# Performance work log

Hardware: AMD Instinct MI355X
Metric: run time of the kernel (lower is better)

The kernel has to match this reference:

```python
import jax, jax.numpy as jnp
import numpy as np

B, S, D, H = 2, 2048, 2048, 16
HD = D // H  # 128
ROPE_BASE = 10000.0


def _rope_tables(seq_len, head_dim, dtype=jnp.float32):
    inv_freq = 1.0 / (ROPE_BASE ** (jnp.arange(0, head_dim, 2, dtype=jnp.float32) / head_dim))
    t = jnp.arange(seq_len, dtype=jnp.float32)
    freqs = jnp.outer(t, inv_freq)  # [S, HD/2]
    # broadcast shape [1, S, 1, HD/2]
    return jnp.cos(freqs)[None, :, None, :].astype(dtype), jnp.sin(freqs)[None, :, None, :].astype(dtype)


def _apply_rope(x, cos, sin):
    # x: [B, S, H, HD]; interleaved split, output concatenated by halves (matches torch code)
    x1 = x[..., ::2]
    x2 = x[..., 1::2]
    return jnp.concatenate([x1 * cos - x2 * sin, x1 * sin + x2 * cos], axis=-1)


def setup_inputs() -> dict:
    key = jax.random.key(0)
    ks = jax.random.split(key, 9)
    xavier = lambda k: jax.random.uniform(k, (D, D), jnp.float32, -1.0, 1.0) * np.sqrt(6.0 / (D + D))
    return {
        "x": jax.random.normal(ks[0], (B, S, D), jnp.float32),
        "attention_mask": jnp.ones((B, S), jnp.int32),
        "wq": xavier(ks[1]), "bq": jnp.zeros((D,), jnp.float32),
        "wk": xavier(ks[2]), "bk": jnp.zeros((D,), jnp.float32),
        "wv": xavier(ks[3]), "bv": jnp.zeros((D,), jnp.float32),
        "wo": xavier(ks[4]), "bo": jnp.zeros((D,), jnp.float32),
    }


def reference(x, attention_mask, wq, bq, wk, bk, wv, bv, wo, bo):
    b, s, _ = x.shape
    scale = HD ** -0.5
    q = (x @ wq + bq).reshape(b, s, H, HD)
    k = (x @ wk + bk).reshape(b, s, H, HD)
    v = (x @ wv + bv).reshape(b, s, H, HD)
    cos, sin = _rope_tables(s, HD, x.dtype)
    q = _apply_rope(q, cos, sin)
    k = _apply_rope(k, cos, sin)
    # [B, H, S, S]
    scores = jnp.einsum('bqhd,bkhd->bhqk', q, k) * scale
    mask = attention_mask[:, None, None, :]  # 2D mask -> [B,1,1,S]
    scores = jnp.where(mask == 0, jnp.asarray(-1e9, scores.dtype), scores)
    attn = jax.nn.softmax(scores, axis=-1)
    out = jnp.einsum('bhqk,bkhd->bqhd', attn, v).reshape(b, s, D)
    return out @ wo + bo
```

## Files before the change

kernel.cpp:

```cpp
#include <hip/hip_runtime.h>

#define Bc 2
#define Sc 2048
#define Dc 2048
#define Hc 16
#define HDc 128
#define Mc 4096

typedef __bf16 bf16_t;
typedef __bf16 bf16x4 __attribute__((ext_vector_type(4)));
typedef __bf16 bf16x8 __attribute__((ext_vector_type(8)));
typedef float f32x4 __attribute__((ext_vector_type(4)));
typedef float f32x16 __attribute__((ext_vector_type(16)));

__device__ __forceinline__ f32x4 mfma16(bf16x8 a, bf16x8 b, f32x4 c) {
  return __builtin_amdgcn_mfma_f32_16x16x32_bf16(a, b, c, 0, 0, 0);
}
__device__ __forceinline__ f32x16 mfma32(bf16x8 a, bf16x8 b, f32x16 c) {
  return __builtin_amdgcn_mfma_f32_32x32x16_bf16(a, b, c, 0, 0, 0);
}

typedef const unsigned __attribute__((address_space(1))) gu32_t;
typedef unsigned __attribute__((address_space(3))) lu32_t;

__device__ __forceinline__ void gload_lds16(const void* g, void* l) {
  gu32_t* gp = (gu32_t*)(unsigned long long)g;
  lu32_t* lp = (lu32_t*)(unsigned)(unsigned long long)l;
  __builtin_amdgcn_global_load_lds(gp, lp, 16, 0, 0);
}

__device__ __forceinline__ unsigned cvtpk(float lo, float hi_) {
  unsigned r;
  asm("v_cvt_pk_bf16_f32 %0, %1, %2" : "=v"(r) : "v"(lo), "v"(hi_));
  return r;
}
__device__ __forceinline__ void plswap(unsigned& a, unsigned& b) {
  asm volatile("v_permlane32_swap_b32 %0, %1" : "+v"(a), "+v"(b));
}

__global__ void cvt_bf16_kernel(const float* __restrict__ in, bf16_t* __restrict__ out, int n4) {
  int i = blockIdx.x * blockDim.x + threadIdx.x;
  if (i < n4) {
    float4 v = ((const float4*)in)[i];
    bf16x4 o;
    o[0] = (bf16_t)v.x; o[1] = (bf16_t)v.y; o[2] = (bf16_t)v.z; o[3] = (bf16_t)v.w;
    ((bf16x4*)out)[i] = o;
  }
}

__global__ void rope_table_kernel(float2* __restrict__ tbl) {
  const int s = blockIdx.x, j = threadIdx.x;
  float freq = expf(-(float)j * (9.210340371976184f / 64.0f));
  float ang = (float)s * freq;
  float sn, cs;
  sincosf(ang, &sn, &cs);
  tbl[s * 64 + j] = make_float2(cs, sn);
}

__global__ void transpose_cvt4_kernel(const float* __restrict__ w0, const float* __restrict__ w1,
                                      const float* __restrict__ w2, const float* __restrict__ w3,
                                      bf16_t* __restrict__ dqkv, bf16_t* __restrict__ dwo) {
  __shared__ float tile[32][33];
  const int z = blockIdx.z;
  const float* w = z == 0 ? w0 : (z == 1 ? w1 : (z == 2 ? w2 : w3));
  bf16_t* wt = z < 3 ? dqkv + (size_t)z * Dc * Dc : dwo;
  const int tx = threadIdx.x, ty = threadIdx.y;
  const int n0 = blockIdx.x * 32, k0 = blockIdx.y * 32;
#pragma unroll
  for (int i = 0; i < 32; i += 8)
    tile[ty + i][tx] = w[(size_t)(k0 + ty + i) * Dc + n0 + tx];
  __syncthreads();
#pragma unroll
  for (int i = 0; i < 32; i += 8)
    wt[(size_t)(n0 + ty + i) * Dc + k0 + tx] = (bf16_t)tile[tx][ty + i];
}

template <int MODE, int NT8>
__global__ __launch_bounds__(512, 1) void gemmp_kernel(
    const bf16_t* __restrict__ A, const bf16_t* __restrict__ Bt,
    const float* __restrict__ bias0, const float* __restrict__ bias1,
    const float* __restrict__ bias2, const float2* __restrict__ tbl,
    void* __restrict__ out0, void* __restrict__ out1, void* __restrict__ out2) {
  __shared__ __align__(16) bf16_t sA[3][256 * 64];
  __shared__ __align__(16) bf16_t sB[3][128 * 64];
  const int tid = threadIdx.x;
  const int lane = tid & 63, wid = tid >> 6;
  const int l15 = lane & 15, g = lane >> 4;
  const int wrow = wid >> 1, wcol = wid & 1;

  const int nwg = 16 * NT8, cpx = nwg / 8;
  const int wgid = ((int)blockIdx.x & 7) * cpx + ((int)blockIdx.x >> 3);
  const int nt = wgid % NT8, mt = wgid / NT8;
  const int m0 = mt * 256, n0 = nt * 128;

  const bf16_t* Ab = A + (size_t)m0 * 2048;
  const bf16_t* Bb = Bt + (size_t)n0 * 2048;

#define GP_STAGE_A(kt, i_)                                           \
  {                                                                  \
    int s_ = (i_) * 512 + tid;                                       \
    int r_ = s_ >> 3;                                                \
    int c_ = ((s_ & 7) ^ (r_ & 7)) * 8;                              \
    gload_lds16(Ab + (size_t)r_ * 2048 + (kt) * 64 + c_,             \
                (char*)&sA[(kt) % 3][0] + s_ * 16);                  \
  }
#define GP_STAGE_B(kt, i_)                                           \
  {                                                                  \
    int s_ = (i_) * 512 + tid;                                       \
    int r_ = s_ >> 3;                                                \
    int c_ = ((s_ & 7) ^ (r_ & 7)) * 8;                              \
    gload_lds16(Bb + (size_t)r_ * 2048 + (kt) * 64 + c_,             \
                (char*)&sB[(kt) % 3][0] + s_ * 16);                  \
  }

  f32x4 acc[4][4] = {};

  GP_STAGE_A(0, 0) GP_STAGE_A(0, 1) GP_STAGE_A(0, 2) GP_STAGE_A(0, 3)
  GP_STAGE_B(0, 0) GP_STAGE_B(0, 1)
  GP_STAGE_A(1, 0) GP_STAGE_A(1, 1) GP_STAGE_A(1, 2) GP_STAGE_A(1, 3)
  GP_STAGE_B(1, 0) GP_STAGE_B(1, 1)

#define GP_BODY(t, DOSTG, VMSTR)                                               \
  {                                                                            \
    asm volatile("s_waitcnt vmcnt(" VMSTR ")" ::: "memory");                   \
    __builtin_amdgcn_s_barrier();                                              \
    __builtin_amdgcn_sched_barrier(0);                                         \
    const char* pA = (const char*)&sA[(t) % 3][0];                             \
    const char* pB = (const char*)&sB[(t) % 3][0];                             \
    bf16x8 af[4][2], bf0[2][2], bf1[2][2];                                     \
    _Pragma("unroll") for (int mi = 0; mi < 4; ++mi)                           \
        _Pragma("unroll") for (int ks = 0; ks < 2; ++ks) {                     \
      int r = wrow * 64 + mi * 16 + l15;                                       \
      af[mi][ks] = *(const bf16x8*)(pA + r * 128 + (((ks * 4 + g) ^ (r & 7)) * 16)); \
    }                                                                          \
    _Pragma("unroll") for (int ni = 0; ni < 2; ++ni)                           \
        _Pragma("unroll") for (int ks = 0; ks < 2; ++ks) {                     \
      int r = wcol * 64 + ni * 16 + l15;                                       \
      bf0[ni][ks] = *(const bf16x8*)(pB + r * 128 + (((ks * 4 + g) ^ (r & 7)) * 16)); \
    }                                                                          \
    if (DOSTG) { GP_STAGE_A((t) + 2, 0) GP_STAGE_A((t) + 2, 1) GP_STAGE_B((t) + 2, 0) } \
    __builtin_amdgcn_s_setprio(1);                                             \
    _Pragma("unroll") for (int mi = 0; mi < 4; ++mi)                           \
        _Pragma("unroll") for (int ni = 0; ni < 2; ++ni)                       \
            _Pragma("unroll") for (int ks = 0; ks < 2; ++ks)                   \
                acc[mi][ni] = mfma16(af[mi][ks], bf0[ni][ks], acc[mi][ni]);    \
    __builtin_amdgcn_s_setprio(0);                                             \
    __builtin_amdgcn_s_barrier();                                              \
    __builtin_amdgcn_sched_barrier(0);                                         \
    _Pragma("unroll") for (int ni = 0; ni < 2; ++ni)                           \
        _Pragma("unroll") for (int ks = 0; ks < 2; ++ks) {                     \
      int r = wcol * 64 + (ni + 2) * 16 + l15;                                 \
      bf1[ni][ks] = *(const bf16x8*)(pB + r * 128 + (((ks * 4 + g) ^ (r & 7)) * 16)); \
    }                                                                          \
    if (DOSTG) { GP_STAGE_A((t) + 2, 2) GP_STAGE_A((t) + 2, 3) GP_STAGE_B((t) + 2, 1) } \
    __builtin_amdgcn_s_setprio(1);                                             \
    _Pragma("unroll") for (int mi = 0; mi < 4; ++mi)                           \
        _Pragma("unroll") for (int ni = 0; ni < 2; ++ni)                       \
            _Pragma("unroll") for (int ks = 0; ks < 2; ++ks)                   \
                acc[mi][ni + 2] = mfma16(af[mi][ks], bf1[ni][ks], acc[mi][ni + 2]); \
    __builtin_amdgcn_s_setprio(0);                                             \
  }

  for (int t = 0; t < 30; ++t) GP_BODY(t, 1, "6");
  GP_BODY(30, 0, "6");
  GP_BODY(31, 0, "0");

#undef GP_BODY
#undef GP_STAGE_A
#undef GP_STAGE_B

  if (MODE == 2) {
#pragma unroll
    for (int mi = 0; mi < 4; ++mi) {
#pragma unroll
      for (int ni = 0; ni < 4; ++ni) {
        const int ncol = n0 + wcol * 64 + ni * 16 + l15;
        const float bv = bias0[ncol];
#pragma unroll
        for (int r = 0; r < 4; ++r) {
          const int mrow = m0 + wrow * 64 + mi * 16 + g * 4 + r;
          ((float*)out0)[(size_t)mrow * 2048 + ncol] = acc[mi][ni][r] + bv;
        }
      }
    }
  } else {
    const int proj = n0 >> 11;
    const float* bp = proj == 0 ? bias0 : (proj == 1 ? bias1 : bias2);
    bf16_t* op = (bf16_t*)(proj == 0 ? out0 : (proj == 1 ? out1 : out2));
#pragma unroll
    for (int mi = 0; mi < 4; ++mi) {
#pragma unroll
      for (int ni = 0; ni < 4; ++ni) {
        const int ncol = n0 + wcol * 64 + ni * 16 + l15;
        const int nloc = ncol & 2047;
        const float bv = bp[nloc];
        const int h = nloc >> 7, hd = nloc & 127;
        if (proj < 2) {
          const int j = hd >> 1;
#pragma unroll
          for (int r = 0; r < 4; ++r) {
            const int mrow = m0 + wrow * 64 + mi * 16 + g * 4 + r;
            const int b = mrow >> 11, sq = mrow & 2047;
            float vv = acc[mi][ni][r] + bv;
            float part = __shfl_xor(vv, 1);
            float2 cn = tbl[(size_t)sq * 64 + j];
            float ov = (l15 & 1) ? (part * cn.y + vv * cn.x)
                                 : (vv * cn.x - part * cn.y);
            op[(((size_t)(b * Hc + h) * Sc + sq) * HDc) + hd] = (bf16_t)ov;
          }
        } else {
#pragma unroll
          for (int r = 0; r < 4; ++r) {
            const int mrow = m0 + wrow * 64 + mi * 16 + g * 4 + r;
            const int b = mrow >> 11, sq = mrow & 2047;
            const float v = acc[mi][ni][r] + bv;
            op[(((size_t)(b * Hc + h) * HDc + hd) * Sc) + sq] = (bf16_t)v;
          }
        }
      }
    }
  }
}

__global__ __launch_bounds__(256, 2) void attn_kernel(
    const bf16_t* __restrict__ Q, const bf16_t* __restrict__ Kr,
    const bf16_t* __restrict__ Vt, const int* __restrict__ mask,
    bf16_t* __restrict__ AO) {
  __shared__ __align__(16) bf16_t sK[2][64 * 128];
  __shared__ __align__(16) bf16_t sV[2][64 * 128];
  __shared__ float mbias[Sc];
  __shared__ float bcast[4][32];
  const int tid = threadIdx.x;
  const int w = tid >> 6, lane = tid & 63;
  const int l31 = lane & 31, hi = lane >> 5;
  const int wbase = w * 64;

  const int bid = blockIdx.x;
  const int L = ((bid & 7) << 6) + (bid >> 3);
  const int qc = L & 15, h = (L >> 4) & 15, b = L >> 8;

  const int* mb = mask + b * Sc;
#pragma unroll
  for (int i = 0; i < Sc / 256; ++i)
    mbias[i * 256 + tid] = mb[i * 256 + tid] ? 0.f : -1e9f;

  const int q0 = qc * 128 + w * 32;
  const bf16_t* qb = Q + ((size_t)(b * Hc + h) * Sc + q0) * HDc;
  const bf16_t* kb = Kr + ((size_t)(b * Hc + h) * Sc) * HDc;
  const bf16_t* vb = Vt + ((size_t)(b * Hc + h) * HDc) * Sc;

  bf16x8 qf[8];
  {
    const bf16_t* qr = qb + (size_t)l31 * HDc + hi * 8;
#pragma unroll
    for (int kk = 0; kk < 8; ++kk) qf[kk] = *(const bf16x8*)(qr + kk * 16);
  }

#define STAGE_KV(sKb, sVb, kv0_)                                             \
  {                                                                          \
    _Pragma("unroll") for (int p = 0; p < 4; ++p) {                          \
      int s_ = p * 256 + tid;                                                \
      int rk = s_ >> 4, ck = s_ & 15;                                        \
      gload_lds16(kb + (size_t)((kv0_) + rk) * HDc + ((ck ^ (rk & 15)) * 8), \
                  (char*)(sKb) + (size_t)(p * 256 + wbase) * 16);            \
      int d63 = s_ >> 4, sv = s_ & 15;                                       \
      int tmp = sv ^ (d63 & 15);                                             \
      int hb = tmp >> 3, cv = tmp & 7;                                       \
      gload_lds16(vb + (size_t)(hb * 64 + d63) * Sc + (kv0_) + cv * 8,       \
                  (char*)(sVb) + (size_t)(p * 256 + wbase) * 16);            \
    }                                                                        \
  }

  bf16_t* sKc = &sK[0][0];
  bf16_t* sKn = &sK[1][0];
  bf16_t* sVc = &sV[0][0];
  bf16_t* sVn = &sV[1][0];

  STAGE_KV(sKc, sVc, 0);
  asm volatile("s_waitcnt vmcnt(0)" ::: "memory");
  __syncthreads();

  f32x16 acc[4];
#pragma unroll
  for (int d = 0; d < 4; ++d) acc[d] = 0.f;
  float mrun = -3.0e38f, lrun = 0.f;
  const float scale = 0.08838834764831845f;

  for (int kv0 = 0; kv0 < Sc; kv0 += 64) {
    if (kv0 + 64 < Sc) STAGE_KV(sKn, sVn, kv0 + 64);

    f32x16 s0 = 0.f, s1 = 0.f;
    {
      const char* kbase = (const char*)sKc;
      __builtin_amdgcn_s_setprio(1);
#pragma unroll
      for (int kk = 0; kk < 8; ++kk) {
        bf16x8 k0f = *(const bf16x8*)(kbase + l31 * 256 + (((2 * kk + hi) ^ (l31 & 15)) * 16));
        bf16x8 k1f = *(const bf16x8*)(kbase + (32 + l31) * 256 + (((2 * kk + hi) ^ ((32 + l31) & 15)) * 16));
        s0 = mfma32(k0f, qf[kk], s0);
        s1 = mfma32(k1f, qf[kk], s1);
      }
      __builtin_amdgcn_s_setprio(0);
    }
    float v[32];
    {
      const float* mp = mbias + kv0 + 4 * hi;
#pragma unroll
      for (int g4 = 0; g4 < 4; ++g4) {
        f32x4 b0 = *(const f32x4*)(mp + 8 * g4);
        f32x4 b1 = *(const f32x4*)(mp + 32 + 8 * g4);
#pragma unroll
        for (int j = 0; j < 4; ++j) {
          v[g4 * 4 + j] = s0[g4 * 4 + j] * scale + b0[j];
          v[16 + g4 * 4 + j] = s1[g4 * 4 + j] * scale + b1[j];
        }
      }
    }
    float tm = v[0];
#pragma unroll
    for (int r = 1; r < 32; ++r) tm = fmaxf(tm, v[r]);
    tm = fmaxf(tm, __shfl_xor(tm, 32));
    if (__any(tm > mrun + 8.f)) {
      float mnew = fmaxf(mrun, tm);
      float al = __expf(mrun - mnew);
      mrun = mnew;
      lrun *= al;
      bcast[w][l31] = al;
      asm volatile("s_waitcnt lgkmcnt(0)" ::: "memory");
      __builtin_amdgcn_sched_barrier(0);
#pragma unroll
      for (int g4 = 0; g4 < 4; ++g4) {
        f32x4 alr = *(const f32x4*)(&bcast[w][8 * g4 + 4 * hi]);
#pragma unroll
        for (int dblk = 0; dblk < 4; ++dblk)
#pragma unroll
          for (int j = 0; j < 4; ++j) acc[dblk][g4 * 4 + j] *= alr[j];
      }
    }
    float ts = 0.f;
#pragma unroll
    for (int r = 0; r < 32; ++r) {
      v[r] = __expf(v[r] - mrun);
      ts += v[r];
    }
    ts += __shfl_xor(ts, 32);
    lrun += ts;
    unsigned pk[4][4];
#pragma unroll
    for (int ks = 0; ks < 4; ++ks) {
      unsigned a1 = cvtpk(v[ks * 8 + 0], v[ks * 8 + 1]);
      unsigned b1 = cvtpk(v[ks * 8 + 4], v[ks * 8 + 5]);
      unsigned a2 = cvtpk(v[ks * 8 + 2], v[ks * 8 + 3]);
      unsigned b2 = cvtpk(v[ks * 8 + 6], v[ks * 8 + 7]);
      plswap(a1, b1);
      plswap(a2, b2);
      pk[ks][0] = a1; pk[ks][1] = a2; pk[ks][2] = b1; pk[ks][3] = b2;
    }
    {
      const char* vbase = (const char*)sVc;
      __builtin_amdgcn_s_setprio(1);
#pragma unroll
      for (int ks = 0; ks < 4; ++ks) {
        bf16x8 pa = *(const bf16x8*)&pk[ks][0];
#pragma unroll
        for (int dblk = 0; dblk < 4; ++dblk) {
          int d = dblk * 32 + l31;
          int slot = (((d >> 6) * 8 + (2 * ks + hi)) ^ (d & 15));
          bf16x8 vf = *(const bf16x8*)(vbase + (d & 63) * 256 + slot * 16);
          acc[dblk] = mfma32(pa, vf, acc[dblk]);
        }
      }
      __builtin_amdgcn_s_setprio(0);
    }
    asm volatile("s_waitcnt vmcnt(0)" ::: "memory");
    __syncthreads();
    bf16_t* t1 = sKc; sKc = sKn; sKn = t1;
    bf16_t* t2 = sVc; sVc = sVn; sVn = t2;
  }

  float inv = 1.f / lrun;
  bcast[w][l31] = inv;
  asm volatile("s_waitcnt lgkmcnt(0)" ::: "memory");
  __builtin_amdgcn_sched_barrier(0);
  bf16_t* ob = AO + ((size_t)b * Sc + q0) * Dc + h * HDc;
#pragma unroll
  for (int g4 = 0; g4 < 4; ++g4) {
    f32x4 ir = *(const f32x4*)(&bcast[w][8 * g4 + 4 * hi]);
#pragma unroll
    for (int j = 0; j < 4; ++j) {
      int q = 8 * g4 + 4 * hi + j;
#pragma unroll
      for (int dblk = 0; dblk < 4; ++dblk)
        ob[(size_t)q * Dc + dblk * 32 + l31] = (bf16_t)(acc[dblk][g4 * 4 + j] * ir[j]);
    }
  }
}

#define MB(x) ((size_t)(x) << 20)

extern "C" void kernel_launch(void* const* d_in, const int* in_sizes, int n_in,
                              void* d_out, int out_size, void* d_ws, size_t ws_size,
                              hipStream_t stream) {
  const float* x = (const float*)d_in[0];
  const int* mask = (const int*)d_in[1];
  const float* wq = (const float*)d_in[2];
  const float* bq = (const float*)d_in[3];
  const float* wk = (const float*)d_in[4];
  const float* bk = (const float*)d_in[5];
  const float* wv = (const float*)d_in[6];
  const float* bv = (const float*)d_in[7];
  const float* wo = (const float*)d_in[8];
  const float* bo = (const float*)d_in[9];
  float* out = (float*)d_out;

  char* ws = (char*)d_ws;
  bf16_t* xb     = (bf16_t*)(ws + MB(0));
  bf16_t* wqkvT  = (bf16_t*)(ws + MB(16));
  bf16_t* woT    = (bf16_t*)(ws + MB(40));
  bf16_t* qbuf   = (bf16_t*)(ws + MB(48));
  bf16_t* kbuf   = (bf16_t*)(ws + MB(64));
  bf16_t* vtb    = (bf16_t*)(ws + MB(80));
  bf16_t* ao     = (bf16_t*)(ws + MB(96));
  float2* rtbl   = (float2*)(ws + MB(112));

  cvt_bf16_kernel<<<8192, 256, 0, stream>>>(x, xb, (Mc * Dc) / 4);
  rope_table_kernel<<<Sc, 64, 0, stream>>>(rtbl);

  dim3 tg(64, 64, 4), tb(32, 8);
  transpose_cvt4_kernel<<<tg, tb, 0, stream>>>(wq, wk, wv, wo, wqkvT, woT);

  gemmp_kernel<0, 48><<<768, 512, 0, stream>>>(xb, wqkvT, bq, bk, bv, rtbl, qbuf, kbuf, vtb);

  attn_kernel<<<Bc * Hc * (Sc / 128), 256, 0, stream>>>(qbuf, kbuf, vtb, mask, ao);

  gemmp_kernel<2, 16><<<256, 512, 0, stream>>>(ao, woT, bo, bo, bo, rtbl, out, out, out);
}
```

Baseline: 270.3 us.

## Process 64 query rows per wave in attention to reuse K/V fragments

Each wave now handles two 32-row query sub-tiles, with two sets of accumulators and separate online-softmax state, so every K and V fragment read from LDS feeds twice as many MFMAs. The block covers 256 queries, which halves the grid and halves the total K/V global and LDS traffic. Launch bounds drop to one block per CU to allow the larger register footprint. The cost is lower occupancy and fewer blocks (256) across the CUs, which reduces latency hiding and may leave some CUs idle.

```diff
diff --git a/kernel.cpp b/kernel.cpp
--- a/kernel.cpp
+++ b/kernel.cpp
@@ -222,7 +222,7 @@
   }
 }
 
-__global__ __launch_bounds__(256, 2) void attn_kernel(
+__global__ __launch_bounds__(256, 1) void attn_kernel(
     const bf16_t* __restrict__ Q, const bf16_t* __restrict__ Kr,
     const bf16_t* __restrict__ Vt, const int* __restrict__ mask,
     bf16_t* __restrict__ AO) {
@@ -236,24 +236,28 @@
   const int wbase = w * 64;
 
   const int bid = blockIdx.x;
-  const int L = ((bid & 7) << 6) + (bid >> 3);
-  const int qc = L & 15, h = (L >> 4) & 15, b = L >> 8;
+  const int L = ((bid & 7) << 5) + (bid >> 3);
+  const int qc = L & 7, h = (L >> 3) & 15, b = L >> 7;
 
   const int* mb = mask + b * Sc;
 #pragma unroll
   for (int i = 0; i < Sc / 256; ++i)
     mbias[i * 256 + tid] = mb[i * 256 + tid] ? 0.f : -1e9f;
 
-  const int q0 = qc * 128 + w * 32;
+  const int q0 = qc * 256 + w * 64;
   const bf16_t* qb = Q + ((size_t)(b * Hc + h) * Sc + q0) * HDc;
   const bf16_t* kb = Kr + ((size_t)(b * Hc + h) * Sc) * HDc;
   const bf16_t* vb = Vt + ((size_t)(b * Hc + h) * HDc) * Sc;
 
-  bf16x8 qf[8];
+  bf16x8 qfA[8], qfB[8];
   {
-    const bf16_t* qr = qb + (size_t)l31 * HDc + hi * 8;
-#pragma unroll
-    for (int kk = 0; kk < 8; ++kk) qf[kk] = *(const bf16x8*)(qr + kk * 16);
+    const bf16_t* qrA = qb + (size_t)l31 * HDc + hi * 8;
+    const bf16_t* qrB = qrA + 32 * HDc;
+#pragma unroll
+    for (int kk = 0; kk < 8; ++kk) {
+      qfA[kk] = *(const bf16x8*)(qrA + kk * 16);
+      qfB[kk] = *(const bf16x8*)(qrB + kk * 16);
+    }
   }
 
 #define STAGE_KV(sKb, sVb, kv0_)                                             \
@@ -280,16 +284,66 @@
   asm volatile("s_waitcnt vmcnt(0)" ::: "memory");
   __syncthreads();
 
-  f32x16 acc[4];
-#pragma unroll
-  for (int d = 0; d < 4; ++d) acc[d] = 0.f;
-  float mrun = -3.0e38f, lrun = 0.f;
+  f32x16 accA[4], accB[4];
+#pragma unroll
+  for (int d = 0; d < 4; ++d) { accA[d] = 0.f; accB[d] = 0.f; }
+  float mrunA = -3.0e38f, lrunA = 0.f;
+  float mrunB = -3.0e38f, lrunB = 0.f;
   const float scale = 0.08838834764831845f;
+
+#define SM_HALF(s0_, s1_, accH, mrunH, lrunH, pkH)                         \
+  {                                                                        \
+    float v[32];                                                           \
+    const float* mp = mbias + kv0 + 4 * hi;                                \
+    _Pragma("unroll") for (int g4 = 0; g4 < 4; ++g4) {                     \
+      f32x4 b0 = *(const f32x4*)(mp + 8 * g4);                             \
+      f32x4 b1 = *(const f32x4*)(mp + 32 + 8 * g4);                        \
+      _Pragma("unroll") for (int j = 0; j < 4; ++j) {                      \
+        v[g4 * 4 + j] = (s0_)[g4 * 4 + j] * scale + b0[j];                 \
+        v[16 + g4 * 4 + j] = (s1_)[g4 * 4 + j] * scale + b1[j];            \
+      }                                                                    \
+    }                                                                      \
+    float tm = v[0];                                                       \
+    _Pragma("unroll") for (int r = 1; r < 32; ++r) tm = fmaxf(tm, v[r]);   \
+    tm = fmaxf(tm, __shfl_xor(tm, 32));                                    \
+    if (__any(tm > (mrunH) + 8.f)) {                                       \
+      float mnew = fmaxf((mrunH), tm);                                     \
+      float al = __expf((mrunH)-mnew);                                     \
+      (mrunH) = mnew;                                                      \
+      (lrunH) *= al;                                                       \
+      bcast[w][l31] = al;                                                  \
+      asm volatile("s_waitcnt lgkmcnt(0)" ::: "memory");                   \
+      __builtin_amdgcn_sched_barrier(0);                                   \
+      _Pragma("unroll") for (int g4 = 0; g4 < 4; ++g4) {                   \
+        f32x4 alr = *(const f32x4*)(&bcast[w][8 * g4 + 4 * hi]);           \
+        _Pragma("unroll") for (int dblk = 0; dblk < 4; ++dblk)             \
+            _Pragma("unroll") for (int j = 0; j < 4; ++j)                  \
+                (accH)[dblk][g4 * 4 + j] *= alr[j];                        \
+      }                                                                    \
+      asm volatile("s_waitcnt lgkmcnt(0)" ::: "memory");                   \
+    }                                                                      \
+    float ts = 0.f;                                                        \
+    _Pragma("unroll") for (int r = 0; r < 32; ++r) {                       \
+      v[r] = __expf(v[r] - (mrunH));                                       \
+      ts += v[r];                                                          \
+    }                                                                      \
+    ts += __shfl_xor(ts, 32);                                              \
+    (lrunH) += ts;                                                         \
+    _Pragma("unroll") for (int ks = 0; ks < 4; ++ks) {                     \
+      unsigned a1 = cvtpk(v[ks * 8 + 0], v[ks * 8 + 1]);                   \
+      unsigned b1 = cvtpk(v[ks * 8 + 4], v[ks * 8 + 5]);                   \
+      unsigned a2 = cvtpk(v[ks * 8 + 2], v[ks * 8 + 3]);                   \
+      unsigned b2 = cvtpk(v[ks * 8 + 6], v[ks * 8 + 7]);                   \
+      plswap(a1, b1);                                                      \
+      plswap(a2, b2);                                                      \
+      pkH[ks][0] = a1; pkH[ks][1] = a2; pkH[ks][2] = b1; pkH[ks][3] = b2;  \
+    }                                                                      \
+  }
 
   for (int kv0 = 0; kv0 < Sc; kv0 += 64) {
     if (kv0 + 64 < Sc) STAGE_KV(sKn, sVn, kv0 + 64);
 
-    f32x16 s0 = 0.f, s1 = 0.f;
+    f32x16 sA0 = 0.f, sA1 = 0.f, sB0 = 0.f, sB1 = 0.f;
     {
       const char* kbase = (const char*)sKc;
       __builtin_amdgcn_s_setprio(1);
@@ -297,77 +351,30 @@
       for (int kk = 0; kk < 8; ++kk) {
         bf16x8 k0f = *(const bf16x8*)(kbase + l31 * 256 + (((2 * kk + hi) ^ (l31 & 15)) * 16));
         bf16x8 k1f = *(const bf16x8*)(kbase + (32 + l31) * 256 + (((2 * kk + hi) ^ ((32 + l31) & 15)) * 16));
-        s0 = mfma32(k0f, qf[kk], s0);
-        s1 = mfma32(k1f, qf[kk], s1);
+        sA0 = mfma32(k0f, qfA[kk], sA0);
+        sA1 = mfma32(k1f, qfA[kk], sA1);
+        sB0 = mfma32(k0f, qfB[kk], sB0);
+        sB1 = mfma32(k1f, qfB[kk], sB1);
       }
       __builtin_amdgcn_s_setprio(0);
     }
-    float v[32];
-    {
-      const float* mp = mbias + kv0 + 4 * hi;
-#pragma unroll
-      for (int g4 = 0; g4 < 4; ++g4) {
-        f32x4 b0 = *(const f32x4*)(mp + 8 * g4);
-        f32x4 b1 = *(const f32x4*)(mp + 32 + 8 * g4);
-#pragma unroll
-        for (int j = 0; j < 4; ++j) {
-          v[g4 * 4 + j] = s0[g4 * 4 + j] * scale + b0[j];
-          v[16 + g4 * 4 + j] = s1[g4 * 4 + j] * scale + b1[j];
-        }
-      }
-    }
-    float tm = v[0];
-#pragma unroll
-    for (int r = 1; r < 32; ++r) tm = fmaxf(tm, v[r]);
-    tm = fmaxf(tm, __shfl_xor(tm, 32));
-    if (__any(tm > mrun + 8.f)) {
-      float mnew = fmaxf(mrun, tm);
-      float al = __expf(mrun - mnew);
-      mrun = mnew;
-      lrun *= al;
-      bcast[w][l31] = al;
-      asm volatile("s_waitcnt lgkmcnt(0)" ::: "memory");
-      __builtin_amdgcn_sched_barrier(0);
-#pragma unroll
-      for (int g4 = 0; g4 < 4; ++g4) {
-        f32x4 alr = *(const f32x4*)(&bcast[w][8 * g4 + 4 * hi]);
-#pragma unroll
-        for (int dblk = 0; dblk < 4; ++dblk)
-#pragma unroll
-          for (int j = 0; j < 4; ++j) acc[dblk][g4 * 4 + j] *= alr[j];
-      }
-    }
-    float ts = 0.f;
-#pragma unroll
-    for (int r = 0; r < 32; ++r) {
-      v[r] = __expf(v[r] - mrun);
-      ts += v[r];
-    }
-    ts += __shfl_xor(ts, 32);
-    lrun += ts;
-    unsigned pk[4][4];
-#pragma unroll
-    for (int ks = 0; ks < 4; ++ks) {
-      unsigned a1 = cvtpk(v[ks * 8 + 0], v[ks * 8 + 1]);
-      unsigned b1 = cvtpk(v[ks * 8 + 4], v[ks * 8 + 5]);
-      unsigned a2 = cvtpk(v[ks * 8 + 2], v[ks * 8 + 3]);
-      unsigned b2 = cvtpk(v[ks * 8 + 6], v[ks * 8 + 7]);
-      plswap(a1, b1);
-      plswap(a2, b2);
-      pk[ks][0] = a1; pk[ks][1] = a2; pk[ks][2] = b1; pk[ks][3] = b2;
-    }
+    unsigned pkA[4][4], pkB[4][4];
+    SM_HALF(sA0, sA1, accA, mrunA, lrunA, pkA);
+    SM_HALF(sB0, sB1, accB, mrunB, lrunB, pkB);
     {
       const char* vbase = (const char*)sVc;
       __builtin_amdgcn_s_setprio(1);
 #pragma unroll
       for (int ks = 0; ks < 4; ++ks) {
-        bf16x8 pa = *(const bf16x8*)&pk[ks][0];
+        bf16x8 paA = *(const bf16x8*)&pkA[ks][0];
+        bf16x8 paB = *(const bf16x8*)&pkB[ks][0];
 #pragma unroll
         for (int dblk = 0; dblk < 4; ++dblk) {
           int d = dblk * 32 + l31;
           int slot = (((d >> 6) * 8 + (2 * ks + hi)) ^ (d & 15));
           bf16x8 vf = *(const bf16x8*)(vbase + (d & 63) * 256 + slot * 16);
-          acc[dblk] = mfma32(pa, vf, acc[dblk]);
+          accA[dblk] = mfma32(paA, vf, accA[dblk]);
+          accB[dblk] = mfma32(paB, vf, accB[dblk]);
         }
       }
       __builtin_amdgcn_s_setprio(0);
@@ -378,21 +385,30 @@
     bf16_t* t2 = sVc; sVc = sVn; sVn = t2;
   }
 
-  float inv = 1.f / lrun;
-  bcast[w][l31] = inv;
-  asm volatile("s_waitcnt lgkmcnt(0)" ::: "memory");
-  __builtin_amdgcn_sched_barrier(0);
+#undef SM_HALF
+#undef STAGE_KV
+
   bf16_t* ob = AO + ((size_t)b * Sc + q0) * Dc + h * HDc;
 #pragma unroll
-  for (int g4 = 0; g4 < 4; ++g4) {
-    f32x4 ir = *(const f32x4*)(&bcast[w][8 * g4 + 4 * hi]);
-#pragma unroll
-    for (int j = 0; j < 4; ++j) {
-      int q = 8 * g4 + 4 * hi + j;
-#pragma unroll
-      for (int dblk = 0; dblk < 4; ++dblk)
-        ob[(size_t)q * Dc + dblk * 32 + l31] = (bf16_t)(acc[dblk][g4 * 4 + j] * ir[j]);
-    }
+  for (int half = 0; half < 2; ++half) {
+    float inv = 1.f / (half == 0 ? lrunA : lrunB);
+    bcast[w][l31] = inv;
+    asm volatile("s_waitcnt lgkmcnt(0)" ::: "memory");
+    __builtin_amdgcn_sched_barrier(0);
+#pragma unroll
+    for (int g4 = 0; g4 < 4; ++g4) {
+      f32x4 ir = *(const f32x4*)(&bcast[w][8 * g4 + 4 * hi]);
+#pragma unroll
+      for (int j = 0; j < 4; ++j) {
+        int q = half * 32 + 8 * g4 + 4 * hi + j;
+#pragma unroll
+        for (int dblk = 0; dblk < 4; ++dblk) {
+          float av = (half == 0 ? accA[dblk][g4 * 4 + j] : accB[dblk][g4 * 4 + j]);
+          ob[(size_t)q * Dc + dblk * 32 + l31] = (bf16_t)(av * ir[j]);
+        }
+      }
+    }
+    asm volatile("s_waitcnt lgkmcnt(0)" ::: "memory");
   }
 }
 
@@ -431,7 +447,7 @@
 
   gemmp_kernel<0, 48><<<768, 512, 0, stream>>>(xb, wqkvT, bq, bk, bv, rtbl, qbuf, kbuf, vtb);
 
-  attn_kernel<<<Bc * Hc * (Sc / 128), 256, 0, stream>>>(qbuf, kbuf, vtb, mask, ao);
+  attn_kernel<<<Bc * Hc * (Sc / 256), 256, 0, stream>>>(qbuf, kbuf, vtb, mask, ao);
 
   gemmp_kernel<2, 16><<<256, 512, 0, stream>>>(ao, woT, bo, bo, bo, rtbl, out, out, out);
 }
```

Result: slower. 289.9 us (+7.2%).
